# Performance work log

Hardware: AMD Instinct MI355X
Metric: run time of the kernel (lower is better)

The kernel has to match this reference:

```python
import jax, jax.numpy as jnp
import numpy as np

NEG_SLOPE = 0.2
EPS = 1e-16


def setup_inputs() -> dict:
    key = jax.random.key(0)
    k1, k2, k3, k4 = jax.random.split(key, 4)
    N, H, F, E = 50000, 4, 32, 800000
    nodes_features = jax.random.normal(k1, (N, H, F), dtype=jnp.float32)
    edge_index = jax.random.randint(k2, (2, E), 0, N, dtype=jnp.int64)
    scoring_fn_source = jax.random.normal(k3, (1, H, F), dtype=jnp.float32)
    scoring_fn_target = jax.random.normal(k4, (1, H, F), dtype=jnp.float32)
    return {
        "nodes_features": nodes_features,
        "scoring_fn_source": scoring_fn_source,
        "scoring_fn_target": scoring_fn_target,
        "edge_index": edge_index,
    }


def reference(nodes_features, scoring_fn_source, scoring_fn_target, edge_index):
    # nodes_features: [N, H, F]; edge_index: [2, E] with row 0 = target, row 1 = source
    num_of_nodes = nodes_features.shape[0]
    trg = edge_index[0]
    src = edge_index[1]

    # Per-node attention logits per head: [N, H]
    scores_source = (nodes_features * scoring_fn_source).sum(axis=-1)
    scores_target = (nodes_features * scoring_fn_target).sum(axis=-1)

    # Lift N -> E via gather: [E, H]
    scores_lifted = scores_source[src] + scores_target[trg]
    src_nodes_features_lifted = nodes_features[src]  # [E, H, F]

    scores_per_edge = jax.nn.leaky_relu(scores_lifted, NEG_SLOPE)
    # Global max subtraction for numerical stability (matches original code)
    scores_per_edge = scores_per_edge - scores_per_edge.max()
    exp_scores = jnp.exp(scores_per_edge)

    # Segment softmax denominator via scatter-add, then gather back per edge
    neighborhood_sums = jax.ops.segment_sum(exp_scores, trg, num_segments=num_of_nodes)
    denom = neighborhood_sums[trg]  # [E, H]

    attentions_per_edge = (exp_scores / (denom + EPS))[..., None]  # [E, H, 1]
    return attentions_per_edge, src_nodes_features_lifted
```

## Files before the change

kernel.cpp:

```cpp
#include <hip/hip_runtime.h>
#include <hip/hip_bf16.h>

#define NEG_SLOPE 0.2f
#define EPSV 1e-16f

typedef float f32x4 __attribute__((ext_vector_type(4)));
typedef float f32x2 __attribute__((ext_vector_type(2)));
typedef short s16x2 __attribute__((ext_vector_type(2)));
typedef unsigned u32x2 __attribute__((ext_vector_type(2)));

__device__ __forceinline__ unsigned fenc(float f) {
    unsigned b = __float_as_uint(f);
    return b ^ ((b & 0x80000000u) ? 0xFFFFFFFFu : 0x80000000u);
}
__device__ __forceinline__ float fdec(unsigned u) {
    unsigned b = (u & 0x80000000u) ? (u ^ 0x80000000u) : ~u;
    return __uint_as_float(b);
}
#define FENC_NEG_INF 0x007FFFFFu

__device__ __forceinline__ unsigned f32_to_bf16_rne(float f) {
    unsigned u = __float_as_uint(f);
    unsigned lsb = (u >> 16) & 1u;
    return (u + 0x7FFFu + lsb) >> 16;
}

__device__ __forceinline__ void pk_atomic_add_bf16(unsigned* addr, float a, float b) {
#if __has_builtin(__builtin_amdgcn_global_atomic_fadd_v2bf16)
    s16x2 v;
    v.x = (short)f32_to_bf16_rne(a);
    v.y = (short)f32_to_bf16_rne(b);
    typedef __attribute__((address_space(1))) s16x2 gs16x2;
    __builtin_amdgcn_global_atomic_fadd_v2bf16((gs16x2*)(void*)addr, v);
#else
    unsigned old = *addr, assumed;
    do {
        assumed = old;
        float lo = __uint_as_float((assumed & 0xFFFFu) << 16) + a;
        float hi = __uint_as_float(assumed & 0xFFFF0000u) + b;
        unsigned nv = (f32_to_bf16_rne(hi) << 16) | (f32_to_bf16_rne(lo) & 0xFFFFu);
        old = atomicCAS(addr, assumed, nv);
    } while (old != assumed);
#endif
}

__global__ void detect_idx_kernel(const unsigned* __restrict__ ei32,
                                  int* __restrict__ flag) {
    __shared__ int anynz;
    if (threadIdx.x == 0) anynz = 0;
    __syncthreads();
    unsigned v = ei32[2 * threadIdx.x + 1];
    if (v != 0u) anynz = 1;
    __syncthreads();
    if (threadIdx.x == 0) *flag = (anynz ? 0 : 1);
}

__device__ __forceinline__ int load_idx(const void* ei, int is64, size_t k) {
    if (is64) return (int)__builtin_nontemporal_load(&((const long long*)ei)[k]);
    return __builtin_nontemporal_load(&((const int*)ei)[k]);
}

__global__ void node_scores_kernel(const float* __restrict__ nf,
                                   const float* __restrict__ sfs,
                                   const float* __restrict__ sft,
                                   float* __restrict__ ss,
                                   float* __restrict__ st,
                                   unsigned* __restrict__ nsum_zero,
                                   unsigned* __restrict__ gmax,
                                   int NH, int nzero) {
    int i = blockIdx.x * blockDim.x + threadIdx.x;
    if (i >= NH) return;
    if (i == 0) *gmax = FENC_NEG_INF;
    for (int k = i; k < nzero; k += NH) nsum_zero[k] = 0u;
    int h = i & 3;
    const float4* __restrict__ row = (const float4*)(nf + (size_t)i * 32);
    const float4* __restrict__ as  = (const float4*)(sfs + h * 32);
    const float4* __restrict__ at  = (const float4*)(sft + h * 32);
    float accs = 0.f, acct = 0.f;
#pragma unroll
    for (int q = 0; q < 8; ++q) {
        float4 v = row[q];
        float4 a = as[q];
        float4 b = at[q];
        accs += v.x * a.x + v.y * a.y + v.z * a.z + v.w * a.w;
        acct += v.x * b.x + v.y * b.y + v.z * b.z + v.w * b.w;
    }
    ss[i] = accs;
    st[i] = acct;
}

__global__ void edge_exp_sum_pk_kernel(const void* __restrict__ ei,
                                       const int* __restrict__ flag,
                                       const float* __restrict__ ss,
                                       const float* __restrict__ st,
                                       float* __restrict__ pbuf,
                                       unsigned* __restrict__ nsum_pk,
                                       unsigned* __restrict__ gmax,
                                       int E) {
    __shared__ float red[256];
    int is64 = *flag;
    int n2 = E * 2;
    int stride = gridDim.x * blockDim.x;
    float lmax = -__builtin_inff();
    for (int i = blockIdx.x * blockDim.x + threadIdx.x; i < n2; i += stride) {
        int e = i >> 1, hp = i & 1;
        int trg = load_idx(ei, is64, e);
        int src = load_idx(ei, is64, (size_t)E + e);
        f32x2 a = *(const f32x2*)(ss + (size_t)src * 4 + hp * 2);
        f32x2 b = *(const f32x2*)(st + (size_t)trg * 4 + hp * 2);
        float s0 = a.x + b.x, s1 = a.y + b.y;
        float lr0 = s0 > 0.f ? s0 : NEG_SLOPE * s0;
        float lr1 = s1 > 0.f ? s1 : NEG_SLOPE * s1;
        lmax = fmaxf(lmax, fmaxf(lr0, lr1));
        float p0 = __expf(lr0), p1 = __expf(lr1);
        f32x2 pv; pv.x = p0; pv.y = p1;
        __builtin_nontemporal_store(pv, (f32x2*)(pbuf + (size_t)e * 4 + hp * 2));
        pk_atomic_add_bf16(nsum_pk + (size_t)trg * 2 + hp, p0, p1);
    }
    red[threadIdx.x] = lmax;
    __syncthreads();
    for (int off = 128; off > 0; off >>= 1) {
        if (threadIdx.x < off)
            red[threadIdx.x] = fmaxf(red[threadIdx.x], red[threadIdx.x + off]);
        __syncthreads();
    }
    if (threadIdx.x == 0) atomicMax(gmax, fenc(red[0]));
}

__global__ void att_pk_kernel(const void* __restrict__ ei,
                              const int* __restrict__ flag,
                              const float* __restrict__ pbuf,
                              const unsigned* __restrict__ nsum_pk,
                              const unsigned* __restrict__ gmax,
                              float* __restrict__ out,
                              int E) {
    int is64 = *flag;
    float de = EPSV * __expf(fdec(*gmax));
    int stride = gridDim.x * blockDim.x;
    for (int e = blockIdx.x * blockDim.x + threadIdx.x; e < E; e += stride) {
        int trg = load_idx(ei, is64, e);
        u32x2 u = *(const u32x2*)(nsum_pk + (size_t)trg * 2);
        f32x4 d;
        d.x = __uint_as_float((u.x & 0xFFFFu) << 16);
        d.y = __uint_as_float(u.x & 0xFFFF0000u);
        d.z = __uint_as_float((u.y & 0xFFFFu) << 16);
        d.w = __uint_as_float(u.y & 0xFFFF0000u);
        f32x4 p = __builtin_nontemporal_load((const f32x4*)(pbuf + (size_t)e * 4));
        f32x4 a = p / (d + de);
        __builtin_nontemporal_store(a, (f32x4*)(out + (size_t)e * 4));
    }
}

__global__ void gather_feat_kernel(const void* __restrict__ ei,
                                   const int* __restrict__ flag,
                                   const f32x4* __restrict__ nf4,
                                   f32x4* __restrict__ out4, int E) {
    int is64 = *flag;
    int n = E * 32;
    int stride = gridDim.x * blockDim.x;
    for (int t = blockIdx.x * blockDim.x + threadIdx.x; t < n; t += stride) {
        int e = t >> 5, q = t & 31;
        int src = load_idx(ei, is64, (size_t)E + e);
        f32x4 v = nf4[(size_t)src * 32 + q];
        __builtin_nontemporal_store(v, &out4[(size_t)e * 32 + q]);
    }
}

__device__ __forceinline__ float edge_lr_rc(const void* ei, int is64,
                                            const float* ss, const float* st,
                                            int E, int e, int h, int* trg_out) {
    int trg = load_idx(ei, is64, e);
    int src = load_idx(ei, is64, (size_t)E + e);
    if (trg_out) *trg_out = trg;
    float s = ss[src * 4 + h] + st[trg * 4 + h];
    return s > 0.f ? s : NEG_SLOPE * s;
}

__global__ void zero_fb_kernel(float* __restrict__ nsum, int n) {
    int i = blockIdx.x * blockDim.x + threadIdx.x;
    if (i < n) nsum[i] = 0.f;
}

__global__ void edge_exp_sum_fb_kernel(const void* __restrict__ ei,
                                       const int* __restrict__ flag,
                                       const float* __restrict__ ss,
                                       const float* __restrict__ st,
                                       float* __restrict__ nsum,
                                       unsigned* __restrict__ gmax, int E) {
    __shared__ float red[256];
    int is64 = *flag;
    int n4 = E * 4;
    int stride = gridDim.x * blockDim.x;
    float lmax = -__builtin_inff();
    for (int i = blockIdx.x * blockDim.x + threadIdx.x; i < n4; i += stride) {
        int trg;
        float lr = edge_lr_rc(ei, is64, ss, st, E, i >> 2, i & 3, &trg);
        lmax = fmaxf(lmax, lr);
        atomicAdd(&nsum[trg * 4 + (i & 3)], __expf(lr));
    }
    red[threadIdx.x] = lmax;
    __syncthreads();
    for (int off = 128; off > 0; off >>= 1) {
        if (threadIdx.x < off)
            red[threadIdx.x] = fmaxf(red[threadIdx.x], red[threadIdx.x + off]);
        __syncthreads();
    }
    if (threadIdx.x == 0) atomicMax(gmax, fenc(red[0]));
}

__global__ void att_fb_kernel(const void* __restrict__ ei,
                              const int* __restrict__ flag,
                              const float* __restrict__ ss,
                              const float* __restrict__ st,
                              const unsigned* __restrict__ gmax,
                              const float* __restrict__ nsum,
                              float* __restrict__ out, int E) {
    int i = blockIdx.x * blockDim.x + threadIdx.x;
    if (i >= E * 4) return;
    int is64 = *flag;
    float de = EPSV * __expf(fdec(*gmax));
    int trg;
    float lr = edge_lr_rc(ei, is64, ss, st, E, i >> 2, i & 3, &trg);
    float a = __expf(lr) / (nsum[trg * 4 + (i & 3)] + de);
    __builtin_nontemporal_store(a, &out[i]);
}

extern "C" void kernel_launch(void* const* d_in, const int* in_sizes, int n_in,
                              void* d_out, int out_size, void* d_ws, size_t ws_size,
                              hipStream_t stream) {
    const float* nf  = (const float*)d_in[0];
    const float* sfs = (const float*)d_in[1];
    const float* sft = (const float*)d_in[2];
    const void*  ei  = d_in[3];

    const int NH = in_sizes[0] / 32;
    const int N  = NH / 4;
    const int E  = in_sizes[3] / 2;

    float* out = (float*)d_out;
    float* ws  = (float*)d_ws;

    float*    ss      = ws;
    float*    st      = ws + NH;
    int*      flag    = (int*)(ws + 2 * (size_t)NH);
    unsigned* gmax    = (unsigned*)(flag + 1);
    float*    pbuf    = ws + 2 * (size_t)NH + 4;
    unsigned* nsum_pk = (unsigned*)(pbuf + (size_t)E * 4);

    size_t need = ((size_t)2 * NH + 4 + (size_t)E * 4 + (size_t)N * 2) * 4;
    bool lean = ws_size >= need;

    const int B = 256;

    detect_idx_kernel<<<1, 256, 0, stream>>>((const unsigned*)ei, flag);

    if (lean) {
        node_scores_kernel<<<(NH + B - 1) / B, B, 0, stream>>>(
            nf, sfs, sft, ss, st, nsum_pk, gmax, NH, N * 2);
        edge_exp_sum_pk_kernel<<<2048, B, 0, stream>>>(ei, flag, ss, st, pbuf,
                                                       nsum_pk, gmax, E);
        att_pk_kernel<<<2048, B, 0, stream>>>(ei, flag, pbuf, nsum_pk, gmax,
                                              out, E);
        gather_feat_kernel<<<4096, B, 0, stream>>>(
            ei, flag, (const f32x4*)nf, (f32x4*)(out + (size_t)E * 4), E);
    } else {
        float* nsum_fb = (float*)(gmax + 1);
        node_scores_kernel<<<(NH + B - 1) / B, B, 0, stream>>>(
            nf, sfs, sft, ss, st, (unsigned*)nsum_fb, gmax, NH, 0);
        zero_fb_kernel<<<(NH + B - 1) / B, B, 0, stream>>>(nsum_fb, NH);
        edge_exp_sum_fb_kernel<<<2048, B, 0, stream>>>(ei, flag, ss, st,
                                                       nsum_fb, gmax, E);
        att_fb_kernel<<<(E * 4 + B - 1) / B, B, 0, stream>>>(ei, flag, ss, st,
                                                             gmax, nsum_fb, out, E);
        gather_feat_kernel<<<4096, B, 0, stream>>>(
            ei, flag, (const f32x4*)nf, (f32x4*)(out + (size_t)E * 4), E);
    }
}
```

Measured before the change: 237.5 us.

## Process whole edges per thread, drop nontemporal loads, widen feature gather

The exp/sum kernel now handles all four heads of an edge in one thread, using float4 loads of the source and target scores and issuing two packed bf16 atomics per edge. Index loads and the pbuf reload switch from nontemporal to ordinary cached loads. The feature gather moves two float4s per thread instead of one. The aim is fewer redundant index loads and better cache reuse, at the cost of more serialized atomics per thread and possibly less parallelism in the exp kernel.

After: 311.3 us. 31.1% more time.

```diff
diff --git a/kernel.cpp b/kernel.cpp
--- a/kernel.cpp
+++ b/kernel.cpp
@@ -1,5 +1,4 @@
 #include <hip/hip_runtime.h>
-#include <hip/hip_bf16.h>
 
 #define NEG_SLOPE 0.2f
 #define EPSV 1e-16f
@@ -56,8 +55,8 @@
 }
 
 __device__ __forceinline__ int load_idx(const void* ei, int is64, size_t k) {
-    if (is64) return (int)__builtin_nontemporal_load(&((const long long*)ei)[k]);
-    return __builtin_nontemporal_load(&((const int*)ei)[k]);
+    if (is64) return (int)((const long long*)ei)[k];
+    return ((const int*)ei)[k];
 }
 
 __global__ void node_scores_kernel(const float* __restrict__ nf,
@@ -89,33 +88,34 @@
     st[i] = acct;
 }
 
-__global__ void edge_exp_sum_pk_kernel(const void* __restrict__ ei,
-                                       const int* __restrict__ flag,
-                                       const float* __restrict__ ss,
-                                       const float* __restrict__ st,
-                                       float* __restrict__ pbuf,
-                                       unsigned* __restrict__ nsum_pk,
-                                       unsigned* __restrict__ gmax,
-                                       int E) {
+__global__ void edge_exp_sum_kernel(const void* __restrict__ ei,
+                                    const int* __restrict__ flag,
+                                    const float* __restrict__ ss,
+                                    const float* __restrict__ st,
+                                    float* __restrict__ pbuf,
+                                    unsigned* __restrict__ nsum_pk,
+                                    unsigned* __restrict__ gmax,
+                                    int E) {
     __shared__ float red[256];
     int is64 = *flag;
-    int n2 = E * 2;
     int stride = gridDim.x * blockDim.x;
     float lmax = -__builtin_inff();
-    for (int i = blockIdx.x * blockDim.x + threadIdx.x; i < n2; i += stride) {
-        int e = i >> 1, hp = i & 1;
+    for (int e = blockIdx.x * blockDim.x + threadIdx.x; e < E; e += stride) {
         int trg = load_idx(ei, is64, e);
         int src = load_idx(ei, is64, (size_t)E + e);
-        f32x2 a = *(const f32x2*)(ss + (size_t)src * 4 + hp * 2);
-        f32x2 b = *(const f32x2*)(st + (size_t)trg * 4 + hp * 2);
-        float s0 = a.x + b.x, s1 = a.y + b.y;
-        float lr0 = s0 > 0.f ? s0 : NEG_SLOPE * s0;
-        float lr1 = s1 > 0.f ? s1 : NEG_SLOPE * s1;
-        lmax = fmaxf(lmax, fmaxf(lr0, lr1));
-        float p0 = __expf(lr0), p1 = __expf(lr1);
-        f32x2 pv; pv.x = p0; pv.y = p1;
-        __builtin_nontemporal_store(pv, (f32x2*)(pbuf + (size_t)e * 4 + hp * 2));
-        pk_atomic_add_bf16(nsum_pk + (size_t)trg * 2 + hp, p0, p1);
+        f32x4 a = *(const f32x4*)(ss + (size_t)src * 4);
+        f32x4 b = *(const f32x4*)(st + (size_t)trg * 4);
+        f32x4 s = a + b;
+        f32x4 p;
+#pragma unroll
+        for (int h = 0; h < 4; ++h) {
+            float lr = s[h] > 0.f ? s[h] : NEG_SLOPE * s[h];
+            lmax = fmaxf(lmax, lr);
+            p[h] = __expf(lr);
+        }
+        *(f32x4*)(pbuf + (size_t)e * 4) = p;
+        pk_atomic_add_bf16(nsum_pk + (size_t)trg * 2 + 0, p[0], p[1]);
+        pk_atomic_add_bf16(nsum_pk + (size_t)trg * 2 + 1, p[2], p[3]);
     }
     red[threadIdx.x] = lmax;
     __syncthreads();
@@ -145,7 +145,7 @@
         d.y = __uint_as_float(u.x & 0xFFFF0000u);
         d.z = __uint_as_float((u.y & 0xFFFFu) << 16);
         d.w = __uint_as_float(u.y & 0xFFFF0000u);
-        f32x4 p = __builtin_nontemporal_load((const f32x4*)(pbuf + (size_t)e * 4));
+        f32x4 p = *(const f32x4*)(pbuf + (size_t)e * 4);
         f32x4 a = p / (d + de);
         __builtin_nontemporal_store(a, (f32x4*)(out + (size_t)e * 4));
     }
@@ -156,13 +156,17 @@
                                    const f32x4* __restrict__ nf4,
                                    f32x4* __restrict__ out4, int E) {
     int is64 = *flag;
-    int n = E * 32;
+    int n = E * 16;
     int stride = gridDim.x * blockDim.x;
     for (int t = blockIdx.x * blockDim.x + threadIdx.x; t < n; t += stride) {
-        int e = t >> 5, q = t & 31;
+        int e = t >> 4, q = (t & 15) * 2;
         int src = load_idx(ei, is64, (size_t)E + e);
-        f32x4 v = nf4[(size_t)src * 32 + q];
-        __builtin_nontemporal_store(v, &out4[(size_t)e * 32 + q]);
+        const f32x4* sp = nf4 + (size_t)src * 32 + q;
+        f32x4 v0 = sp[0];
+        f32x4 v1 = sp[1];
+        f32x4* dp = out4 + (size_t)e * 32 + q;
+        __builtin_nontemporal_store(v0, dp);
+        __builtin_nontemporal_store(v1, dp + 1);
     }
 }
 
@@ -257,8 +261,8 @@
     if (lean) {
         node_scores_kernel<<<(NH + B - 1) / B, B, 0, stream>>>(
             nf, sfs, sft, ss, st, nsum_pk, gmax, NH, N * 2);
-        edge_exp_sum_pk_kernel<<<2048, B, 0, stream>>>(ei, flag, ss, st, pbuf,
-                                                       nsum_pk, gmax, E);
+        edge_exp_sum_kernel<<<2048, B, 0, stream>>>(ei, flag, ss, st, pbuf,
+                                                    nsum_pk, gmax, E);
         att_pk_kernel<<<2048, B, 0, stream>>>(ei, flag, pbuf, nsum_pk, gmax,
                                               out, E);
         gather_feat_kernel<<<4096, B, 0, stream>>>(
```
